# Performance work log

Hardware: AMD Instinct MI355X
Metric: run time of the kernel (lower is better)

## Reference

```python
import jax, jax.numpy as jnp
import numpy as np

D = 2          # qudit dimension
L = 22         # number of qudits; state length = D**L = 4194304
INDEX = tuple(range(L))  # rotation applied on every qudit (angle[i] indexed by qudit position)

# Generator S = Sx(j=0, k=1) on a D-level system: |0><1| + |1><0|
def _make_S():
    S = np.zeros((D, D), dtype=np.complex64)
    S[0, 1] = 1.0
    S[1, 0] = 1.0
    return jnp.asarray(S)


def setup_inputs() -> dict:
    key = jax.random.key(0)
    k1, k2, k3 = jax.random.split(key, 3)
    n = D ** L
    x_real = jax.random.normal(k1, (n,), dtype=jnp.float32)
    x_imag = jax.random.normal(k2, (n,), dtype=jnp.float32)
    angle = jax.random.uniform(k3, (L,), dtype=jnp.float32)
    return {"x_real": x_real, "x_imag": x_imag, "angle": angle}


def reference(x_real, x_imag, angle):
    # U = kron_i expm(-0.5j * angle[i] * S)  (identity on qudits not in INDEX),
    # applied as U @ x. Instead of materializing the D^L x D^L sparse unitary,
    # apply each single-qudit gate by contracting axis i of the reshaped state,
    # which is exactly the same linear map.
    S = _make_S()
    psi = (x_real + 1j * x_imag).astype(jnp.complex64).reshape((D,) * L)
    for i in range(L):
        if i in INDEX:
            M = jax.scipy.linalg.expm((-0.5j) * angle[i].astype(jnp.complex64) * S)
            # contract qudit axis i: psi'[..., a, ...] = sum_b M[a,b] psi[..., b, ...]
            psi = jnp.moveaxis(jnp.tensordot(M, psi, axes=([1], [i])), 0, i)
        # else: identity, nothing to do
    out = psi.reshape(-1)
    return jnp.stack([out.real, out.imag])  # (2, D**L) float32
```

## Files before the change

kernel.cpp:

```cpp
#include <hip/hip_runtime.h>


constexpr int NTOT = 1 << 22;

__device__ __forceinline__ void rotg(float& ar, float& ai, float& br, float& bi,
                                     float c, float s) {
    float t0 = ar, t1 = ai, t2 = br, t3 = bi;
    ar = fmaf(c, t0,  s * t3);
    ai = fmaf(c, t1, -s * t2);
    br = fmaf(c, t2,  s * t1);
    bi = fmaf(c, t3, -s * t0);
}

__device__ __forceinline__ void build_cs(const float* __restrict__ ang,
                                         float* cs_c, float* cs_s, int t) {
    if (t < 22) {
        float a = 0.5f * ang[21 - t];
        cs_c[t] = cosf(a);
        cs_s[t] = sinf(a);
    }
}

__global__ __launch_bounds__(256) void rgate_low(const float* __restrict__ xr,
                                                 const float* __restrict__ xi,
                                                 const float* __restrict__ ang,
                                                 float* __restrict__ out) {
    __shared__ float sr[2304];
    __shared__ float si[2304];
    __shared__ float cs_c[22], cs_s[22];
    const int t  = threadIdx.x;
    const int g0 = blockIdx.x << 11;

    build_cs(ang, cs_c, cs_s, t);

    float ar[8], ai[8];
    {
        const float4* xr4 = (const float4*)(xr + g0) + 2 * t;
        const float4* xi4 = (const float4*)(xi + g0) + 2 * t;
        float4 a0 = xr4[0], a1 = xr4[1];
        float4 b0 = xi4[0], b1 = xi4[1];
        ar[0]=a0.x; ar[1]=a0.y; ar[2]=a0.z; ar[3]=a0.w;
        ar[4]=a1.x; ar[5]=a1.y; ar[6]=a1.z; ar[7]=a1.w;
        ai[0]=b0.x; ai[1]=b0.y; ai[2]=b0.z; ai[3]=b0.w;
        ai[4]=b1.x; ai[5]=b1.y; ai[6]=b1.z; ai[7]=b1.w;
    }
    __syncthreads();

    #pragma unroll
    for (int k = 0; k < 3; ++k) {
        const int m = 1 << k;
        const float c = cs_c[k], s = cs_s[k];
        #pragma unroll
        for (int j = 0; j < 8; ++j)
            if (!(j & m)) rotg(ar[j], ai[j], ar[j|m], ai[j|m], c, s);
    }
    #pragma unroll
    for (int j = 0; j < 8; ++j) { sr[9*t + j] = ar[j]; si[9*t + j] = ai[j]; }
    __syncthreads();

    {
        const int base = 72 * (t >> 3) + (t & 7);
        #pragma unroll
        for (int j = 0; j < 8; ++j) { ar[j] = sr[base + 9*j]; ai[j] = si[base + 9*j]; }
        #pragma unroll
        for (int k = 3; k < 6; ++k) {
            const int m = 1 << (k - 3);
            const float c = cs_c[k], s = cs_s[k];
            #pragma unroll
            for (int j = 0; j < 8; ++j)
                if (!(j & m)) rotg(ar[j], ai[j], ar[j|m], ai[j|m], c, s);
        }
        #pragma unroll
        for (int j = 0; j < 8; ++j) { sr[base + 9*j] = ar[j]; si[base + 9*j] = ai[j]; }
    }
    __syncthreads();

    {
        const int lo2  = t & 63;
        const int base = 576 * (t >> 6) + lo2 + (lo2 >> 3);
        #pragma unroll
        for (int j = 0; j < 8; ++j) { ar[j] = sr[base + 72*j]; ai[j] = si[base + 72*j]; }
        #pragma unroll
        for (int k = 6; k < 9; ++k) {
            const int m = 1 << (k - 6);
            const float c = cs_c[k], s = cs_s[k];
            #pragma unroll
            for (int j = 0; j < 8; ++j)
                if (!(j & m)) rotg(ar[j], ai[j], ar[j|m], ai[j|m], c, s);
        }
        #pragma unroll
        for (int j = 0; j < 8; ++j) { sr[base + 72*j] = ar[j]; si[base + 72*j] = ai[j]; }
    }
    __syncthreads();

    #pragma unroll
    for (int grp = 0; grp < 2; ++grp) {
        const int lo3  = t + (grp << 8);
        const int base = lo3 + (lo3 >> 3);
        float br_[4], bi_[4];
        #pragma unroll
        for (int j = 0; j < 4; ++j) { br_[j] = sr[base + 576*j]; bi_[j] = si[base + 576*j]; }
        {
            const float c9 = cs_c[9], s9 = cs_s[9];
            rotg(br_[0], bi_[0], br_[1], bi_[1], c9, s9);
            rotg(br_[2], bi_[2], br_[3], bi_[3], c9, s9);
            const float c10 = cs_c[10], s10 = cs_s[10];
            rotg(br_[0], bi_[0], br_[2], bi_[2], c10, s10);
            rotg(br_[1], bi_[1], br_[3], bi_[3], c10, s10);
        }
        #pragma unroll
        for (int j = 0; j < 4; ++j) {
            out[g0 + lo3 + 512*j]        = br_[j];
            out[NTOT + g0 + lo3 + 512*j] = bi_[j];
        }
    }
}

__global__ __launch_bounds__(256) void rgate_mid(const float* __restrict__ ang,
                                                 float* __restrict__ out) {
    __shared__ float sr[2048], si[2048];
    __shared__ float cs_c[22], cs_s[22];
    const int t    = threadIdx.x;
    const int bid  = blockIdx.x;
    const int base = ((bid >> 5) << 16) + ((bid & 31) << 6);
    float* outr = out;
    float* outi = out + NTOT;

    build_cs(ang, cs_c, cs_s, t);

    #pragma unroll
    for (int e = 0; e < 8; ++e) {
        const int f = e * 256 + t;
        const int g = base + ((f >> 6) << 11) + (f & 63);
        sr[f] = outr[g]; si[f] = outi[g];
    }
    __syncthreads();

    #pragma unroll
    for (int gg = 0; gg < 5; ++gg) {
        const int   sh = 1 << gg;
        const float c  = cs_c[11 + gg], s = cs_s[11 + gg];
        #pragma unroll
        for (int e = 0; e < 4; ++e) {
            const int p  = e * 256 + t;
            const int lo = p & 63, hp = p >> 6;
            const int hl = hp & (sh - 1);
            const int ha = ((hp - hl) << 1) + hl;
            const int sa = (ha << 6) + lo;
            const int sb = sa + (sh << 6);
            rotg(sr[sa], si[sa], sr[sb], si[sb], c, s);
        }
        __syncthreads();
    }

    #pragma unroll
    for (int e = 0; e < 8; ++e) {
        const int f = e * 256 + t;
        const int g = base + ((f >> 6) << 11) + (f & 63);
        outr[g] = sr[f]; outi[g] = si[f];
    }
}

__global__ __launch_bounds__(256) void rgate_high(const float* __restrict__ ang,
                                                  float* __restrict__ out) {
    __shared__ float sr[2048], si[2048];
    __shared__ float cs_c[22], cs_s[22];
    const int t    = threadIdx.x;
    const int l0   = blockIdx.x << 5;
    float* outr = out;
    float* outi = out + NTOT;

    build_cs(ang, cs_c, cs_s, t);

    #pragma unroll
    for (int e = 0; e < 8; ++e) {
        const int f = e * 256 + t;
        const int g = ((f >> 5) << 16) + l0 + (f & 31);
        sr[f] = outr[g]; si[f] = outi[g];
    }
    __syncthreads();

    #pragma unroll
    for (int gg = 0; gg < 6; ++gg) {
        const int   sh = 1 << gg;
        const float c  = cs_c[16 + gg], s = cs_s[16 + gg];
        #pragma unroll
        for (int e = 0; e < 4; ++e) {
            const int p  = e * 256 + t;
            const int lo = p & 31, hp = p >> 5;
            const int hl = hp & (sh - 1);
            const int ha = ((hp - hl) << 1) + hl;
            const int sa = (ha << 5) + lo;
            const int sb = sa + (sh << 5);
            rotg(sr[sa], si[sa], sr[sb], si[sb], c, s);
        }
        __syncthreads();
    }

    #pragma unroll
    for (int e = 0; e < 8; ++e) {
        const int f = e * 256 + t;
        const int g = ((f >> 5) << 16) + l0 + (f & 31);
        outr[g] = sr[f]; outi[g] = si[f];
    }
}

extern "C" void kernel_launch(void* const* d_in, const int* in_sizes, int n_in,
                              void* d_out, int out_size, void* d_ws, size_t ws_size,
                              hipStream_t stream) {
    const float* xr  = (const float*)d_in[0];
    const float* xi  = (const float*)d_in[1];
    const float* ang = (const float*)d_in[2];
    float* out = (float*)d_out;

    rgate_low<<<2048, 256, 0, stream>>>(xr, xi, ang, out);
    rgate_mid<<<2048, 256, 0, stream>>>(ang, out);
    rgate_high<<<2048, 256, 0, stream>>>(ang, out);
}
```

Baseline: 120.9 us.

## Repartition qubit passes 12/5/5 with register-level butterflies and fewer shared-memory rounds

The low kernel now handles 12 qubits per 4096-element block, using 16 values per thread and three register-butterfly phases joined by padded interleaved float2 shared-memory transposes. The mid and high kernels each take 5 qubits. They run 3 butterflies in registers straight after the global loads and 2 more after one shared-memory exchange, replacing the five or six shared-memory read-modify-write rounds with barriers. The aim is to cut shared-memory traffic and barrier count while keeping global access coalesced. The cost is higher register pressure and a new launch configuration with 1024 blocks for the low kernel.

```diff
diff --git a/kernel.cpp b/kernel.cpp
--- a/kernel.cpp
+++ b/kernel.cpp
@@ -21,187 +21,196 @@
     }
 }
 
-__global__ __launch_bounds__(256) void rgate_low(const float* __restrict__ xr,
-                                                 const float* __restrict__ xi,
-                                                 const float* __restrict__ ang,
-                                                 float* __restrict__ out) {
-    __shared__ float sr[2304];
-    __shared__ float si[2304];
+__device__ __forceinline__ int padslot(int i) { return i + (i >> 4) + (i >> 8); }
+
+__global__ __launch_bounds__(256, 4) void rgate_low(const float* __restrict__ xr,
+                                                    const float* __restrict__ xi,
+                                                    const float* __restrict__ ang,
+                                                    float* __restrict__ out) {
+    __shared__ float2 sv[4368];
     __shared__ float cs_c[22], cs_s[22];
     const int t  = threadIdx.x;
-    const int g0 = blockIdx.x << 11;
+    const int g0 = blockIdx.x << 12;
 
     build_cs(ang, cs_c, cs_s, t);
 
-    float ar[8], ai[8];
+    float ar[16], ai[16];
+    const float* xrp = xr + g0 + t;
+    const float* xip = xi + g0 + t;
+    #pragma unroll
+    for (int j = 0; j < 16; ++j) {
+        ar[j] = xrp[j << 8];
+        ai[j] = xip[j << 8];
+    }
+    __syncthreads();
+
+    #pragma unroll
+    for (int b = 0; b < 4; ++b) {
+        const int m = 1 << b;
+        const float c = cs_c[8 + b], s = cs_s[8 + b];
+        #pragma unroll
+        for (int j = 0; j < 16; ++j)
+            if (!(j & m)) rotg(ar[j], ai[j], ar[j | m], ai[j | m], c, s);
+    }
+    #pragma unroll
+    for (int j = 0; j < 16; ++j)
+        sv[padslot(t + (j << 8))] = make_float2(ar[j], ai[j]);
+    __syncthreads();
+
     {
-        const float4* xr4 = (const float4*)(xr + g0) + 2 * t;
-        const float4* xi4 = (const float4*)(xi + g0) + 2 * t;
-        float4 a0 = xr4[0], a1 = xr4[1];
-        float4 b0 = xi4[0], b1 = xi4[1];
-        ar[0]=a0.x; ar[1]=a0.y; ar[2]=a0.z; ar[3]=a0.w;
-        ar[4]=a1.x; ar[5]=a1.y; ar[6]=a1.z; ar[7]=a1.w;
-        ai[0]=b0.x; ai[1]=b0.y; ai[2]=b0.z; ai[3]=b0.w;
-        ai[4]=b1.x; ai[5]=b1.y; ai[6]=b1.z; ai[7]=b1.w;
-    }
-    __syncthreads();
-
-    #pragma unroll
-    for (int k = 0; k < 3; ++k) {
-        const int m = 1 << k;
-        const float c = cs_c[k], s = cs_s[k];
-        #pragma unroll
-        for (int j = 0; j < 8; ++j)
-            if (!(j & m)) rotg(ar[j], ai[j], ar[j|m], ai[j|m], c, s);
-    }
-    #pragma unroll
-    for (int j = 0; j < 8; ++j) { sr[9*t + j] = ar[j]; si[9*t + j] = ai[j]; }
+        const int base2 = (t & 15) + ((t >> 4) << 8);
+        #pragma unroll
+        for (int j = 0; j < 16; ++j) {
+            float2 v = sv[padslot(base2 + (j << 4))];
+            ar[j] = v.x; ai[j] = v.y;
+        }
+        #pragma unroll
+        for (int b = 0; b < 4; ++b) {
+            const int m = 1 << b;
+            const float c = cs_c[4 + b], s = cs_s[4 + b];
+            #pragma unroll
+            for (int j = 0; j < 16; ++j)
+                if (!(j & m)) rotg(ar[j], ai[j], ar[j | m], ai[j | m], c, s);
+        }
+        #pragma unroll
+        for (int j = 0; j < 16; ++j)
+            sv[padslot(base2 + (j << 4))] = make_float2(ar[j], ai[j]);
+    }
     __syncthreads();
 
     {
-        const int base = 72 * (t >> 3) + (t & 7);
-        #pragma unroll
-        for (int j = 0; j < 8; ++j) { ar[j] = sr[base + 9*j]; ai[j] = si[base + 9*j]; }
-        #pragma unroll
-        for (int k = 3; k < 6; ++k) {
-            const int m = 1 << (k - 3);
-            const float c = cs_c[k], s = cs_s[k];
+        const int base3 = t << 4;
+        #pragma unroll
+        for (int j = 0; j < 16; ++j) {
+            float2 v = sv[padslot(base3 + j)];
+            ar[j] = v.x; ai[j] = v.y;
+        }
+        #pragma unroll
+        for (int b = 0; b < 4; ++b) {
+            const int m = 1 << b;
+            const float c = cs_c[b], s = cs_s[b];
             #pragma unroll
-            for (int j = 0; j < 8; ++j)
-                if (!(j & m)) rotg(ar[j], ai[j], ar[j|m], ai[j|m], c, s);
-        }
-        #pragma unroll
-        for (int j = 0; j < 8; ++j) { sr[base + 9*j] = ar[j]; si[base + 9*j] = ai[j]; }
-    }
-    __syncthreads();
-
-    {
-        const int lo2  = t & 63;
-        const int base = 576 * (t >> 6) + lo2 + (lo2 >> 3);
-        #pragma unroll
-        for (int j = 0; j < 8; ++j) { ar[j] = sr[base + 72*j]; ai[j] = si[base + 72*j]; }
-        #pragma unroll
-        for (int k = 6; k < 9; ++k) {
-            const int m = 1 << (k - 6);
-            const float c = cs_c[k], s = cs_s[k];
-            #pragma unroll
-            for (int j = 0; j < 8; ++j)
-                if (!(j & m)) rotg(ar[j], ai[j], ar[j|m], ai[j|m], c, s);
-        }
-        #pragma unroll
-        for (int j = 0; j < 8; ++j) { sr[base + 72*j] = ar[j]; si[base + 72*j] = ai[j]; }
-    }
-    __syncthreads();
-
-    #pragma unroll
-    for (int grp = 0; grp < 2; ++grp) {
-        const int lo3  = t + (grp << 8);
-        const int base = lo3 + (lo3 >> 3);
-        float br_[4], bi_[4];
-        #pragma unroll
-        for (int j = 0; j < 4; ++j) { br_[j] = sr[base + 576*j]; bi_[j] = si[base + 576*j]; }
-        {
-            const float c9 = cs_c[9], s9 = cs_s[9];
-            rotg(br_[0], bi_[0], br_[1], bi_[1], c9, s9);
-            rotg(br_[2], bi_[2], br_[3], bi_[3], c9, s9);
-            const float c10 = cs_c[10], s10 = cs_s[10];
-            rotg(br_[0], bi_[0], br_[2], bi_[2], c10, s10);
-            rotg(br_[1], bi_[1], br_[3], bi_[3], c10, s10);
-        }
-        #pragma unroll
-        for (int j = 0; j < 4; ++j) {
-            out[g0 + lo3 + 512*j]        = br_[j];
-            out[NTOT + g0 + lo3 + 512*j] = bi_[j];
+            for (int j = 0; j < 16; ++j)
+                if (!(j & m)) rotg(ar[j], ai[j], ar[j | m], ai[j | m], c, s);
+        }
+        float4* orp = (float4*)(out + g0 + base3);
+        float4* oip = (float4*)(out + NTOT + g0 + base3);
+        #pragma unroll
+        for (int q = 0; q < 4; ++q) {
+            orp[q] = make_float4(ar[4*q], ar[4*q+1], ar[4*q+2], ar[4*q+3]);
+            oip[q] = make_float4(ai[4*q], ai[4*q+1], ai[4*q+2], ai[4*q+3]);
         }
     }
 }
 
 __global__ __launch_bounds__(256) void rgate_mid(const float* __restrict__ ang,
                                                  float* __restrict__ out) {
-    __shared__ float sr[2048], si[2048];
+    __shared__ float2 sv[2048];
     __shared__ float cs_c[22], cs_s[22];
     const int t    = threadIdx.x;
+    const int lane = t & 63, w = t >> 6;
     const int bid  = blockIdx.x;
-    const int base = ((bid >> 5) << 16) + ((bid & 31) << 6);
+    const int base = ((bid >> 6) << 17) + ((bid & 63) << 6) + lane;
     float* outr = out;
     float* outi = out + NTOT;
 
     build_cs(ang, cs_c, cs_s, t);
 
-    #pragma unroll
-    for (int e = 0; e < 8; ++e) {
-        const int f = e * 256 + t;
-        const int g = base + ((f >> 6) << 11) + (f & 63);
-        sr[f] = outr[g]; si[f] = outi[g];
-    }
-    __syncthreads();
-
-    #pragma unroll
-    for (int gg = 0; gg < 5; ++gg) {
-        const int   sh = 1 << gg;
-        const float c  = cs_c[11 + gg], s = cs_s[11 + gg];
-        #pragma unroll
-        for (int e = 0; e < 4; ++e) {
-            const int p  = e * 256 + t;
-            const int lo = p & 63, hp = p >> 6;
-            const int hl = hp & (sh - 1);
-            const int ha = ((hp - hl) << 1) + hl;
-            const int sa = (ha << 6) + lo;
-            const int sb = sa + (sh << 6);
-            rotg(sr[sa], si[sa], sr[sb], si[sb], c, s);
-        }
-        __syncthreads();
-    }
-
-    #pragma unroll
-    for (int e = 0; e < 8; ++e) {
-        const int f = e * 256 + t;
-        const int g = base + ((f >> 6) << 11) + (f & 63);
-        outr[g] = sr[f]; outi[g] = si[f];
+    float ar[8], ai[8];
+    #pragma unroll
+    for (int j = 0; j < 8; ++j) {
+        const int g = base + ((j | (w << 3)) << 12);
+        ar[j] = outr[g]; ai[j] = outi[g];
+    }
+    __syncthreads();
+
+    #pragma unroll
+    for (int b = 0; b < 3; ++b) {
+        const int m = 1 << b;
+        const float c = cs_c[12 + b], s = cs_s[12 + b];
+        #pragma unroll
+        for (int j = 0; j < 8; ++j)
+            if (!(j & m)) rotg(ar[j], ai[j], ar[j | m], ai[j | m], c, s);
+    }
+    #pragma unroll
+    for (int j = 0; j < 8; ++j)
+        sv[((j | (w << 3)) << 6) + lane] = make_float2(ar[j], ai[j]);
+    __syncthreads();
+
+    #pragma unroll
+    for (int j = 0; j < 8; ++j) {
+        const int h = ((j & 3) << 3) | (w << 1) | (j >> 2);
+        float2 v = sv[(h << 6) + lane];
+        ar[j] = v.x; ai[j] = v.y;
+    }
+    #pragma unroll
+    for (int b = 0; b < 2; ++b) {
+        const int m = 1 << b;
+        const float c = cs_c[15 + b], s = cs_s[15 + b];
+        #pragma unroll
+        for (int j = 0; j < 8; ++j)
+            if (!(j & m)) rotg(ar[j], ai[j], ar[j | m], ai[j | m], c, s);
+    }
+    #pragma unroll
+    for (int j = 0; j < 8; ++j) {
+        const int h = ((j & 3) << 3) | (w << 1) | (j >> 2);
+        const int g = base + (h << 12);
+        outr[g] = ar[j]; outi[g] = ai[j];
     }
 }
 
 __global__ __launch_bounds__(256) void rgate_high(const float* __restrict__ ang,
                                                   float* __restrict__ out) {
-    __shared__ float sr[2048], si[2048];
+    __shared__ float2 sv[2048];
     __shared__ float cs_c[22], cs_s[22];
     const int t    = threadIdx.x;
-    const int l0   = blockIdx.x << 5;
+    const int lane = t & 63, w = t >> 6;
+    const int base = (blockIdx.x << 6) + lane;
     float* outr = out;
     float* outi = out + NTOT;
 
     build_cs(ang, cs_c, cs_s, t);
 
-    #pragma unroll
-    for (int e = 0; e < 8; ++e) {
-        const int f = e * 256 + t;
-        const int g = ((f >> 5) << 16) + l0 + (f & 31);
-        sr[f] = outr[g]; si[f] = outi[g];
-    }
-    __syncthreads();
-
-    #pragma unroll
-    for (int gg = 0; gg < 6; ++gg) {
-        const int   sh = 1 << gg;
-        const float c  = cs_c[16 + gg], s = cs_s[16 + gg];
-        #pragma unroll
-        for (int e = 0; e < 4; ++e) {
-            const int p  = e * 256 + t;
-            const int lo = p & 31, hp = p >> 5;
-            const int hl = hp & (sh - 1);
-            const int ha = ((hp - hl) << 1) + hl;
-            const int sa = (ha << 5) + lo;
-            const int sb = sa + (sh << 5);
-            rotg(sr[sa], si[sa], sr[sb], si[sb], c, s);
-        }
-        __syncthreads();
-    }
-
-    #pragma unroll
-    for (int e = 0; e < 8; ++e) {
-        const int f = e * 256 + t;
-        const int g = ((f >> 5) << 16) + l0 + (f & 31);
-        outr[g] = sr[f]; outi[g] = si[f];
+    float ar[8], ai[8];
+    #pragma unroll
+    for (int j = 0; j < 8; ++j) {
+        const int g = ((j | (w << 3)) << 17) + base;
+        ar[j] = outr[g]; ai[j] = outi[g];
+    }
+    __syncthreads();
+
+    #pragma unroll
+    for (int b = 0; b < 3; ++b) {
+        const int m = 1 << b;
+        const float c = cs_c[17 + b], s = cs_s[17 + b];
+        #pragma unroll
+        for (int j = 0; j < 8; ++j)
+            if (!(j & m)) rotg(ar[j], ai[j], ar[j | m], ai[j | m], c, s);
+    }
+    #pragma unroll
+    for (int j = 0; j < 8; ++j)
+        sv[((j | (w << 3)) << 6) + lane] = make_float2(ar[j], ai[j]);
+    __syncthreads();
+
+    #pragma unroll
+    for (int j = 0; j < 8; ++j) {
+        const int u = ((j & 3) << 3) | (w << 1) | (j >> 2);
+        float2 v = sv[(u << 6) + lane];
+        ar[j] = v.x; ai[j] = v.y;
+    }
+    #pragma unroll
+    for (int b = 0; b < 2; ++b) {
+        const int m = 1 << b;
+        const float c = cs_c[20 + b], s = cs_s[20 + b];
+        #pragma unroll
+        for (int j = 0; j < 8; ++j)
+            if (!(j & m)) rotg(ar[j], ai[j], ar[j | m], ai[j | m], c, s);
+    }
+    #pragma unroll
+    for (int j = 0; j < 8; ++j) {
+        const int u = ((j & 3) << 3) | (w << 1) | (j >> 2);
+        const int g = (u << 17) + base;
+        outr[g] = ar[j]; outi[g] = ai[j];
     }
 }
 
@@ -213,7 +222,7 @@
     const float* ang = (const float*)d_in[2];
     float* out = (float*)d_out;
 
-    rgate_low<<<2048, 256, 0, stream>>>(xr, xi, ang, out);
+    rgate_low<<<1024, 256, 0, stream>>>(xr, xi, ang, out);
     rgate_mid<<<2048, 256, 0, stream>>>(ang, out);
     rgate_high<<<2048, 256, 0, stream>>>(ang, out);
 }
```

After: 113.0 us. 1.07x faster.
